# Optimization experiments

Hardware: AMD Instinct MI355X
Metric: run time of the kernel (lower is better)

The kernel has to match this reference:

```python
import jax, jax.numpy as jnp
import numpy as np

B, T, E, D, A, H, C, K = 32, 1500, 512, 512, 512, 4, 10, 201
SHARPENING = 1.0


def setup_inputs() -> dict:
    key = jax.random.key(0)
    ks = jax.random.split(key, 11)
    def w(k, shape, fan_in):
        return jax.random.normal(k, shape, jnp.float32) / np.sqrt(fan_in).astype(np.float32)
    return {
        "enc_out": jax.random.normal(ks[0], (B, T, E), jnp.float32),
        "x_lens": jax.random.randint(ks[1], (B,), T // 2, T + 1),
        "dec_out": jax.random.normal(ks[2], (B, 1, D), jnp.float32),
        # previous-step attention weights: a valid distribution over T per head
        "aw_step": jax.nn.softmax(jax.random.normal(ks[3], (B, T, H), jnp.float32), axis=1),
        "w_enc": w(ks[4], (H, E, A), E),   # per-head LinearND(enc->att)
        "b_enc": jnp.zeros((H, A), jnp.float32),
        "w_dec": w(ks[5], (H, D, A), D),   # per-head LinearND(dec->att), no bias
        "w_conv": w(ks[6], (H, C, A), C),  # per-head LinearND(conv_ch->att), no bias
        "conv_k": w(ks[7], (H * C, 1, K), K),  # grouped 1D conv kernels (O,I,K), groups=H
        "v": w(ks[8], (H, A), A),          # per-head LinearND(att->1), no bias
        "w_mha": w(ks[9], (H * E, E), H * E),
        "b_mha": jnp.zeros((E,), jnp.float32),
    }


def reference(enc_out, x_lens, dec_out, aw_step, w_enc, b_enc, w_dec, w_conv, conv_k, v, w_mha, b_mha):
    b, t, e = enc_out.shape
    h = aw_step.shape[-1]
    c = w_conv.shape[1]
    k = conv_k.shape[-1]
    # enc_out_a: per-head encoder projection [B,T,H,A]
    enc_a = jnp.einsum('bte,hea->btha', enc_out, w_enc) + b_enc
    # decoder projection, broadcast over time [B,1,H,A]
    dec_a = jnp.einsum('bd,hda->bha', dec_out[:, 0], w_dec)[:, None]
    # location features: grouped 1D conv over previous attention weights
    aw_t = jnp.transpose(aw_step, (0, 2, 1))  # [B,H,T]
    conv = jax.lax.conv_general_dilated(
        aw_t, conv_k, window_strides=(1,), padding=[(k // 2, k // 2)],
        dimension_numbers=('NCH', 'OIH', 'NCH'), feature_group_count=h)  # [B,H*C,T]
    conv = conv.reshape(b, h, c, t).transpose(0, 3, 1, 2)  # [B,T,H,C]
    conv_a = jnp.einsum('bthc,hca->btha', conv, w_conv)
    # additive energy [B,T,H]
    energy = jnp.einsum('btha,ha->bth', jnp.tanh(enc_a + dec_a + conv_a), v)
    # original code multiplies energy by mask (1 valid, -1024 padded) then sharpening
    mask = jnp.where(jnp.arange(t)[None, :] < x_lens[:, None], 1.0, -1024.0).astype(energy.dtype)
    energy = energy * mask[:, :, None] * SHARPENING
    aw = jax.nn.softmax(energy, axis=1)  # softmax over time per head
    # per-head context, concatenated along feature dim -> [B,1,H*E]
    ctx = jnp.einsum('bte,bth->bhe', enc_out, aw).reshape(b, 1, h * e)
    ctx = ctx @ w_mha + b_mha  # [B,1,E]
    return ctx, aw
```

## Files before the change

kernel.cpp:

```cpp
#include <hip/hip_runtime.h>
#include <hip/hip_bf16.h>

#define BB 32
#define TT 1500
#define TP 1536
#define EE 512
#define HH 4
#define AA 512
#define NN 2048
#define CC 10
#define KCONV 201
#define KAUG 576

typedef __attribute__((ext_vector_type(8))) __bf16 bf16x8;
typedef __attribute__((ext_vector_type(4))) float f32x4;

__device__ __forceinline__ unsigned short f2bf(float x) {
    unsigned int u = __float_as_uint(x);
    u = (u + 0x7fffu + ((u >> 16) & 1u)) >> 16;
    return (unsigned short)u;
}
__device__ __forceinline__ float bf2f(unsigned short u) {
    return __uint_as_float(((unsigned int)u) << 16);
}
__device__ __forceinline__ void glds16(const void* g, void* l) {
    __builtin_amdgcn_global_load_lds(
        (const __attribute__((address_space(1))) unsigned int*)g,
        (__attribute__((address_space(3))) unsigned int*)l, 16, 0, 0);
}
__device__ __forceinline__ float tanh_fast(float x) {
    float e = __expf(x * 2.0f);
    return fmaf(-2.0f, __builtin_amdgcn_rcpf(e + 1.0f), 1.0f);
}

#define PREP_DEC0   0
#define PREP_CONV0  1024
#define PREP_WT0    8704
#define PREP_PAD0   13312
#define PREP_ENC0   20404
#define PREP_TOTAL  44404

__global__ __launch_bounds__(256) void k_prep(
    const float* __restrict__ enc, const int* __restrict__ xl,
    const float* __restrict__ dec_out, const float* __restrict__ aw_step,
    const float* __restrict__ w_enc, const float* __restrict__ b_enc,
    const float* __restrict__ w_dec, const float* __restrict__ w_conv,
    const float* __restrict__ conv_k,
    unsigned short* __restrict__ Whi, unsigned short* __restrict__ Wlo,
    unsigned short* __restrict__ Ahi, unsigned short* __restrict__ Alo,
    float* __restrict__ dec_a) {
    __shared__ float sbuf[456 + KCONV];
    const int bid = blockIdx.x;
    const int tid = threadIdx.x;

    if (bid < PREP_CONV0) {
        const int b  = bid >> 5;
        const int n0 = (bid & 31) * 64;
        const int n  = n0 + (tid & 63);
        const int dg = tid >> 6;
        const int h  = n >> 9, a = n & 511;
        const float* dp = dec_out + (size_t)b * 512 + dg * 128;
        const float* wp = w_dec + ((size_t)h * 512 + dg * 128) * 512 + a;
        float acc = 0.f;
#pragma unroll 8
        for (int d = 0; d < 128; ++d) acc += dp[d] * wp[(size_t)d * 512];
        sbuf[tid] = acc;
        __syncthreads();
        if (tid < 64) {
            float tot = sbuf[tid] + sbuf[tid + 64] + sbuf[tid + 128] + sbuf[tid + 192];
            dec_a[(size_t)b * NN + n0 + tid] = b_enc[n0 + tid] + tot;
        }
    } else if (bid < PREP_WT0) {
        int r = bid - PREP_CONV0;
        const int tch = r % 6;
        const int hc  = (r / 6) % 40;
        const int b   = r / 240;
        const int h   = hc / 10;
        const int t0  = tch * 256;
        float* sAw = sbuf;
        float* sK  = sbuf + 456;
        for (int i = tid; i < 456; i += 256) {
            int ts = t0 - 100 + i;
            sAw[i] = (ts >= 0 && ts < TT) ? aw_step[((size_t)b * TT + ts) * HH + h] : 0.f;
        }
        if (tid < KCONV) sK[tid] = conv_k[(size_t)hc * KCONV + tid];
        __syncthreads();
        int t = t0 + tid;
        if (t < TT) {
            float acc = 0.f;
            for (int k = 0; k < KCONV; ++k) acc += sAw[tid + k] * sK[k];
            size_t o = ((size_t)b * TP + t) * KAUG + 512 + hc;
            unsigned short hi = f2bf(acc);
            Ahi[o] = hi; Alo[o] = f2bf(acc - bf2f(hi));
        }
    } else if (bid < PREP_PAD0) {
        int idx = (bid - PREP_WT0) * 256 + tid;
        int n = idx / KAUG, k = idx % KAUG;
        int h = n >> 9, a = n & 511;
        float val = 0.f;
        if (k < 512) {
            val = w_enc[((size_t)h * 512 + k) * 512 + a];
        } else if (k < 552) {
            int j = k - 512; int h2 = j / 10, c = j % 10;
            if (h2 == h) val = w_conv[((size_t)h * 10 + c) * 512 + a];
        }
        unsigned short hi = f2bf(val);
        Whi[idx] = hi;
        Wlo[idx] = f2bf(val - bf2f(hi));
    } else if (bid < PREP_ENC0) {
        int idx = (bid - PREP_PAD0) * 256 + tid;
        const int tot1 = BB * 36 * KAUG;
        const int tot2 = BB * TT * 24;
        size_t o;
        if (idx < tot1) {
            int b = idx / (36 * KAUG); int r2 = idx % (36 * KAUG);
            int t = 1500 + r2 / KAUG;  int k = r2 % KAUG;
            o = ((size_t)b * TP + t) * KAUG + k;
        } else if (idx < tot1 + tot2) {
            int j = idx - tot1;
            int b = j / (TT * 24); int r2 = j % (TT * 24);
            int t = r2 / 24;       int k = 552 + r2 % 24;
            o = ((size_t)b * TP + t) * KAUG + k;
        } else return;
        Ahi[o] = 0; Alo[o] = 0;
    } else {
        long idx = (long)(bid - PREP_ENC0) * 256 + tid;
        if (idx >= 6144000L) return;
        long f = idx * 4;
        int b = (int)(f / 768000);
        int r2 = (int)(f % 768000);
        int t = r2 >> 9, e = r2 & 511;
        float4 vv = *reinterpret_cast<const float4*>(enc + f);
        ushort4 h4;
        h4.x = f2bf(vv.x); h4.y = f2bf(vv.y); h4.z = f2bf(vv.z); h4.w = f2bf(vv.w);
        size_t o = ((size_t)b * TP + t) * KAUG + e;
        *reinterpret_cast<ushort4*>(Ahi + o) = h4;
        if (((t & ~127) + 128) > xl[b]) {
            ushort4 l4;
            l4.x = f2bf(vv.x - bf2f(h4.x));
            l4.y = f2bf(vv.y - bf2f(h4.y));
            l4.z = f2bf(vv.z - bf2f(h4.z));
            l4.w = f2bf(vv.w - bf2f(h4.w));
            *reinterpret_cast<ushort4*>(Alo + o) = l4;
        }
    }
}

__global__ __launch_bounds__(256, 3) void k_gemm(
    const unsigned short* __restrict__ Ahi, const unsigned short* __restrict__ Alo,
    const unsigned short* __restrict__ Whi, const unsigned short* __restrict__ Wlo,
    const float* __restrict__ dec_a, const float* __restrict__ vvec,
    const int* __restrict__ xl, float* __restrict__ energy) {
    __shared__ unsigned short lsA[3][4096];
    __shared__ unsigned short lsB[3][4096];
    const int bid = blockIdx.x;
    const int g = ((bid >> 7) << 3) + (bid & 7);
    const int ntile = (bid >> 3) & 15;
    const int b = g / 12, mtile = g % 12;
    const int m0 = mtile * 128, n0 = ntile * 128;
    const int xlen = xl[b];
    const int nk = (m0 + 128 <= xlen) ? 18 : 54;

    const int tid = threadIdx.x;
    const int lane = tid & 63, wave = tid >> 6;
    const int wm = wave >> 1, wn = wave & 1;

    f32x4 acc[4][4];
#pragma unroll
    for (int i = 0; i < 4; i++)
#pragma unroll
        for (int j = 0; j < 4; j++) acc[i][j] = (f32x4){0.f, 0.f, 0.f, 0.f};

    const int row = tid >> 2;
    const int ko  = ((tid & 3) ^ ((tid >> 3) & 3)) * 8;
    const size_t abase = ((size_t)b * TP + m0 + row) * KAUG + ko;
    const size_t bbase = ((size_t)n0 + row) * KAUG + ko;
    const int l1 = tid * 8;
    const int l2 = l1 + 2048;
    const int ar = wm * 64, br = wn * 64;
    const int fo = (lane & 15) * 32 + (((lane >> 4) ^ ((lane >> 1) & 3)) * 8);

    auto stage = [&](int t, int buf) {
        const int seg = (t >= 36) ? 2 : ((t >= 18) ? 1 : 0);
        const int k0 = (t - seg * 18) * 32;
        const unsigned short* Ap = (seg == 2) ? Alo : Ahi;
        const unsigned short* Bp = (seg == 1) ? Wlo : Whi;
        glds16(Ap + abase + k0,                     &lsA[buf][l1]);
        glds16(Ap + abase + k0 + (size_t)64 * KAUG, &lsA[buf][l2]);
        glds16(Bp + bbase + k0,                     &lsB[buf][l1]);
        glds16(Bp + bbase + k0 + (size_t)64 * KAUG, &lsB[buf][l2]);
    };
    auto compute = [&](int buf) {
        bf16x8 ah[4], bh[4];
#pragma unroll
        for (int i = 0; i < 4; i++) {
            ah[i] = *(const bf16x8*)&lsA[buf][(ar + i * 16) * 32 + fo];
            bh[i] = *(const bf16x8*)&lsB[buf][(br + i * 16) * 32 + fo];
        }
        __builtin_amdgcn_s_setprio(1);
#pragma unroll
        for (int i = 0; i < 4; i++)
#pragma unroll
            for (int j = 0; j < 4; j++)
                acc[i][j] = __builtin_amdgcn_mfma_f32_16x16x32_bf16(ah[i], bh[j], acc[i][j], 0, 0, 0);
        __builtin_amdgcn_s_setprio(0);
    };

    stage(0, 0);
    stage(1, 1);
    int bc = 0, bp = 2;
    for (int t = 0; t < nk - 1; ++t) {
        asm volatile("s_waitcnt vmcnt(4)" ::: "memory");
        __builtin_amdgcn_s_barrier();
        __builtin_amdgcn_sched_barrier(0);
        if (t + 2 < nk) stage(t + 2, bp);
        __builtin_amdgcn_sched_barrier(0);
        compute(bc);
        __builtin_amdgcn_sched_barrier(0);
        bc = (bc == 2) ? 0 : bc + 1;
        bp = (bp == 2) ? 0 : bp + 1;
    }
    asm volatile("s_waitcnt vmcnt(0)" ::: "memory");
    __builtin_amdgcn_s_barrier();
    __builtin_amdgcn_sched_barrier(0);
    compute(bc);

    const int h = ntile >> 2;
    const int kg = lane >> 4;
    float dv[4], vv[4];
#pragma unroll
    for (int j = 0; j < 4; j++) {
        int ng = n0 + wn * 64 + j * 16 + (lane & 15);
        dv[j] = dec_a[(size_t)b * NN + ng];
        vv[j] = vvec[ng];
    }
#pragma unroll
    for (int i = 0; i < 4; i++) {
        float part[4] = {0.f, 0.f, 0.f, 0.f};
#pragma unroll
        for (int j = 0; j < 4; j++)
#pragma unroll
            for (int r = 0; r < 4; r++)
                part[r] += tanh_fast(acc[i][j][r] + dv[j]) * vv[j];
#pragma unroll
        for (int r = 0; r < 4; r++) {
            float s = part[r];
            s += __shfl_xor(s, 1, 64);
            s += __shfl_xor(s, 2, 64);
            s += __shfl_xor(s, 4, 64);
            s += __shfl_xor(s, 8, 64);
            if ((lane & 15) == 0) {
                int t = m0 + wm * 64 + i * 16 + kg * 4 + r;
                if (t < TT)
                    atomicAdd(&energy[((size_t)b * HH + h) * TP + t], s);
            }
        }
    }
}

__global__ __launch_bounds__(512) void k_softmax(const float* __restrict__ energy,
                                                 const int* __restrict__ x_lens,
                                                 float* __restrict__ aw) {
    const int b = blockIdx.x >> 2, h = blockIdx.x & 3;
    const int tid = threadIdx.x;
    __shared__ float sE[TT];
    __shared__ float red[512];
    const int xlen = x_lens[b];
    float lmax = -3.4e38f;
    for (int t = tid; t < TT; t += 512) {
        float e = energy[((size_t)b * HH + h) * TP + t];
        float m = (t < xlen) ? e : e * -1024.0f;
        sE[t] = m;
        lmax = fmaxf(lmax, m);
    }
    red[tid] = lmax; __syncthreads();
    for (int s = 256; s > 0; s >>= 1) { if (tid < s) red[tid] = fmaxf(red[tid], red[tid + s]); __syncthreads(); }
    float mx = red[0]; __syncthreads();
    float lsum = 0.f;
    for (int t = tid; t < TT; t += 512) {
        float ex = expf(sE[t] - mx);
        sE[t] = ex; lsum += ex;
    }
    red[tid] = lsum; __syncthreads();
    for (int s = 256; s > 0; s >>= 1) { if (tid < s) red[tid] += red[tid + s]; __syncthreads(); }
    float sum = red[0];
    for (int t = tid; t < TT; t += 512)
        aw[((size_t)b * TT + t) * HH + h] = sE[t] / sum;
}

__global__ __launch_bounds__(512) void k_ctx(const float* __restrict__ enc,
                                             const float* __restrict__ aw,
                                             float* __restrict__ ctx_h) {
    const int chunk = blockIdx.x, b = blockIdx.y;
    const int t0 = chunk * 64;
    const int nt = (TT - t0 < 64) ? (TT - t0) : 64;
    __shared__ float sA[64 * 4];
    const int tid = threadIdx.x;
    for (int i = tid; i < nt * 4; i += 512)
        sA[i] = aw[((size_t)b * TT + t0) * HH + i];
    __syncthreads();
    float a0 = 0.f, a1 = 0.f, a2 = 0.f, a3 = 0.f;
    const float* ep = enc + ((size_t)b * TT + t0) * EE + tid;
    if (nt == 64) {
#pragma unroll 8
        for (int tt = 0; tt < 64; ++tt) {
            float ev = ep[(size_t)tt * EE];
            a0 += sA[tt * 4 + 0] * ev; a1 += sA[tt * 4 + 1] * ev;
            a2 += sA[tt * 4 + 2] * ev; a3 += sA[tt * 4 + 3] * ev;
        }
    } else {
        for (int tt = 0; tt < nt; ++tt) {
            float ev = ep[(size_t)tt * EE];
            a0 += sA[tt * 4 + 0] * ev; a1 += sA[tt * 4 + 1] * ev;
            a2 += sA[tt * 4 + 2] * ev; a3 += sA[tt * 4 + 3] * ev;
        }
    }
    atomicAdd(&ctx_h[((size_t)b * HH + 0) * EE + tid], a0);
    atomicAdd(&ctx_h[((size_t)b * HH + 1) * EE + tid], a1);
    atomicAdd(&ctx_h[((size_t)b * HH + 2) * EE + tid], a2);
    atomicAdd(&ctx_h[((size_t)b * HH + 3) * EE + tid], a3);
}

__global__ __launch_bounds__(256) void k_mha(const float* __restrict__ ctx_h,
                                             const float* __restrict__ w_mha,
                                             const float* __restrict__ b_mha,
                                             float* __restrict__ out) {
    __shared__ float sred[256];
    const int tid = threadIdx.x;
    const int b  = blockIdx.x >> 2;
    const int eo = ((blockIdx.x & 3) << 7) + (tid & 127);
    const int kg = tid >> 7;
    const float* c = ctx_h + (size_t)b * NN + kg * 1024;
    const float* w = w_mha + ((size_t)kg * 1024) * EE + eo;
    float acc = 0.f;
#pragma unroll 8
    for (int k = 0; k < 1024; ++k) acc += c[k] * w[(size_t)k * EE];
    sred[tid] = acc;
    __syncthreads();
    if (tid < 128)
        out[(size_t)b * EE + eo] = b_mha[eo] + sred[tid] + sred[tid + 128];
}

extern "C" void kernel_launch(void* const* d_in, const int* in_sizes, int n_in,
                              void* d_out, int out_size, void* d_ws, size_t ws_size,
                              hipStream_t stream) {
    (void)in_sizes; (void)n_in; (void)out_size;
    const float* enc    = (const float*)d_in[0];
    const int*   xlen   = (const int*)d_in[1];
    const float* dec    = (const float*)d_in[2];
    const float* aw_in  = (const float*)d_in[3];
    const float* w_enc  = (const float*)d_in[4];
    const float* b_enc  = (const float*)d_in[5];
    const float* w_dec  = (const float*)d_in[6];
    const float* w_conv = (const float*)d_in[7];
    const float* convk  = (const float*)d_in[8];
    const float* v      = (const float*)d_in[9];
    const float* w_mha  = (const float*)d_in[10];
    const float* b_mha  = (const float*)d_in[11];
    float* out = (float*)d_out;

    char* ws = (char*)d_ws;
    unsigned short* Whi = (unsigned short*)ws;
    unsigned short* Wlo = Whi + (size_t)NN * KAUG;
    unsigned short* Ahi = (unsigned short*)(ws + 4718592);
    unsigned short* Alo = Ahi + (size_t)BB * TP * KAUG;
    float* dec_a  = (float*)(ws + 117964800);
    float* energy = (float*)(ws + 118226944);
    float* ctx_h  = (float*)(ws + 119013376);
    (void)ws_size;

    hipMemsetAsync(energy, 0, 786432 + 262144, stream);

    k_prep<<<dim3(PREP_TOTAL), 256, 0, stream>>>(enc, xlen, dec, aw_in, w_enc, b_enc,
                                                 w_dec, w_conv, convk,
                                                 Whi, Wlo, Ahi, Alo, dec_a);
    k_gemm<<<dim3(6144), 256, 0, stream>>>(Ahi, Alo, Whi, Wlo, dec_a, v, xlen, energy);
    k_softmax<<<dim3(BB * HH), 512, 0, stream>>>(energy, xlen, out + 16384);
    k_ctx <<<dim3(24, BB), 512, 0, stream>>>(enc, out + 16384, ctx_h);
    k_mha <<<dim3(128), 256, 0, stream>>>(ctx_h, w_mha, b_mha, out);
}
```

Measured before the change: 595.2 us.

## Enlarge GEMM tiles to 256x256 with 8 waves and interleaved loads

The energy GEMM moves from 128x128 tiles with 4 waves to 256x256 tiles with 512 threads, so each wave holds an 8x4 block of MFMA accumulators. The K-loop is restructured so the global-to-LDS stages are spread between four MFMA phases rather than issued as one batch, and block order is remapped so heavy tail tiles (the last M tiles) are scheduled first. The low-precision correction region widens from 128-row to 256-row granularity, so more rows take the 54-step path. Fewer blocks and more data reuse per tile are traded against higher register/LDS pressure, lower occupancy and more wasted work on partial tiles.

Measured after the change: 623.4 us. 1.05x slower.

```diff
diff --git a/kernel.cpp b/kernel.cpp
--- a/kernel.cpp
+++ b/kernel.cpp
@@ -135,7 +135,7 @@
         h4.x = f2bf(vv.x); h4.y = f2bf(vv.y); h4.z = f2bf(vv.z); h4.w = f2bf(vv.w);
         size_t o = ((size_t)b * TP + t) * KAUG + e;
         *reinterpret_cast<ushort4*>(Ahi + o) = h4;
-        if (((t & ~127) + 128) > xl[b]) {
+        if (((t & ~255) + 256) > xl[b]) {
             ushort4 l4;
             l4.x = f2bf(vv.x - bf2f(h4.x));
             l4.y = f2bf(vv.y - bf2f(h4.y));
@@ -146,86 +146,112 @@
     }
 }
 
-__global__ __launch_bounds__(256, 3) void k_gemm(
+__global__ __launch_bounds__(512, 2) void k_gemm(
     const unsigned short* __restrict__ Ahi, const unsigned short* __restrict__ Alo,
     const unsigned short* __restrict__ Whi, const unsigned short* __restrict__ Wlo,
     const float* __restrict__ dec_a, const float* __restrict__ vvec,
     const int* __restrict__ xl, float* __restrict__ energy) {
-    __shared__ unsigned short lsA[3][4096];
-    __shared__ unsigned short lsB[3][4096];
+    __shared__ unsigned short lsA[3][8192];
+    __shared__ unsigned short lsB[3][8192];
     const int bid = blockIdx.x;
-    const int g = ((bid >> 7) << 3) + (bid & 7);
-    const int ntile = (bid >> 3) & 15;
-    const int b = g / 12, mtile = g % 12;
-    const int m0 = mtile * 128, n0 = ntile * 128;
+    const int ntile = bid & 7;
+    const int rest = bid >> 3;
+    const int mtile = 5 - (rest >> 5);
+    const int b = rest & 31;
+    const int m0 = mtile * 256, n0 = ntile * 256;
     const int xlen = xl[b];
-    const int nk = (m0 + 128 <= xlen) ? 18 : 54;
+    const int nk = (m0 + 256 <= xlen) ? 18 : 54;
 
     const int tid = threadIdx.x;
     const int lane = tid & 63, wave = tid >> 6;
-    const int wm = wave >> 1, wn = wave & 1;
-
-    f32x4 acc[4][4];
-#pragma unroll
-    for (int i = 0; i < 4; i++)
+    const int wm = wave >> 2, wn = wave & 3;
+
+    f32x4 acc[8][4];
+#pragma unroll
+    for (int i = 0; i < 8; i++)
 #pragma unroll
         for (int j = 0; j < 4; j++) acc[i][j] = (f32x4){0.f, 0.f, 0.f, 0.f};
 
-    const int row = tid >> 2;
-    const int ko  = ((tid & 3) ^ ((tid >> 3) & 3)) * 8;
-    const size_t abase = ((size_t)b * TP + m0 + row) * KAUG + ko;
-    const size_t bbase = ((size_t)n0 + row) * KAUG + ko;
-    const int l1 = tid * 8;
-    const int l2 = l1 + 2048;
-    const int ar = wm * 64, br = wn * 64;
-    const int fo = (lane & 15) * 32 + (((lane >> 4) ^ ((lane >> 1) & 3)) * 8);
-
-    auto stage = [&](int t, int buf) {
-        const int seg = (t >= 36) ? 2 : ((t >= 18) ? 1 : 0);
-        const int k0 = (t - seg * 18) * 32;
-        const unsigned short* Ap = (seg == 2) ? Alo : Ahi;
-        const unsigned short* Bp = (seg == 1) ? Wlo : Whi;
-        glds16(Ap + abase + k0,                     &lsA[buf][l1]);
-        glds16(Ap + abase + k0 + (size_t)64 * KAUG, &lsA[buf][l2]);
-        glds16(Bp + bbase + k0,                     &lsB[buf][l1]);
-        glds16(Bp + bbase + k0 + (size_t)64 * KAUG, &lsB[buf][l2]);
-    };
-    auto compute = [&](int buf) {
-        bf16x8 ah[4], bh[4];
-#pragma unroll
-        for (int i = 0; i < 4; i++) {
-            ah[i] = *(const bf16x8*)&lsA[buf][(ar + i * 16) * 32 + fo];
-            bh[i] = *(const bf16x8*)&lsB[buf][(br + i * 16) * 32 + fo];
-        }
-        __builtin_amdgcn_s_setprio(1);
-#pragma unroll
-        for (int i = 0; i < 4; i++)
-#pragma unroll
-            for (int j = 0; j < 4; j++)
-                acc[i][j] = __builtin_amdgcn_mfma_f32_16x16x32_bf16(ah[i], bh[j], acc[i][j], 0, 0, 0);
-        __builtin_amdgcn_s_setprio(0);
-    };
-
-    stage(0, 0);
-    stage(1, 1);
-    int bc = 0, bp = 2;
-    for (int t = 0; t < nk - 1; ++t) {
-        asm volatile("s_waitcnt vmcnt(4)" ::: "memory");
-        __builtin_amdgcn_s_barrier();
-        __builtin_amdgcn_sched_barrier(0);
-        if (t + 2 < nk) stage(t + 2, bp);
-        __builtin_amdgcn_sched_barrier(0);
-        compute(bc);
-        __builtin_amdgcn_sched_barrier(0);
-        bc = (bc == 2) ? 0 : bc + 1;
-        bp = (bp == 2) ? 0 : bp + 1;
-    }
-    asm volatile("s_waitcnt vmcnt(0)" ::: "memory");
+    const int r = tid >> 2;
+    const int rowP2 = r + (r & 64);
+    const int ko = ((tid & 3) ^ ((r >> 1) & 3)) * 8;
+    const size_t abase = ((size_t)b * TP + m0 + rowP2) * KAUG + ko;
+    const size_t bbase = ((size_t)n0 + r) * KAUG + ko;
+    const int ldstA = rowP2 * 32 + (tid & 3) * 8;
+    const int ldstB = tid * 8;
+    const int fc = ((lane >> 4) ^ ((lane >> 1) & 3)) * 8;
+    const int arow0 = wm * 128 + (lane & 15);
+    const int brow0 = wn * 64 + (lane & 15);
+
+#define STG0(BUF, BP, K0) glds16((BP) + bbase + (K0), &lsB[BUF][ldstB])
+#define STG1(BUF, BP, K0) glds16((BP) + bbase + (size_t)128 * KAUG + (K0), &lsB[BUF][ldstB + 4096])
+#define STG2(BUF, AP, K0) glds16((AP) + abase + (K0), &lsA[BUF][ldstA])
+#define STG3(BUF, AP, K0) glds16((AP) + abase + (size_t)64 * KAUG + (K0), &lsA[BUF][ldstA + 2048])
+#define MFMA4(AF, AI) \
+    acc[AI][0] = __builtin_amdgcn_mfma_f32_16x16x32_bf16(AF, bfr0, acc[AI][0], 0, 0, 0); \
+    acc[AI][1] = __builtin_amdgcn_mfma_f32_16x16x32_bf16(AF, bfr1, acc[AI][1], 0, 0, 0); \
+    acc[AI][2] = __builtin_amdgcn_mfma_f32_16x16x32_bf16(AF, bfr2, acc[AI][2], 0, 0, 0); \
+    acc[AI][3] = __builtin_amdgcn_mfma_f32_16x16x32_bf16(AF, bfr3, acc[AI][3], 0, 0, 0);
+#define PHASE(P) { \
+    bf16x8 a0 = *(const bf16x8*)&lA[(arow0 + (2 * (P)) * 16) * 32 + fc]; \
+    bf16x8 a1 = *(const bf16x8*)&lA[(arow0 + (2 * (P) + 1) * 16) * 32 + fc]; \
+    __builtin_amdgcn_s_setprio(1); \
+    MFMA4(a0, 2 * (P)); \
+    MFMA4(a1, 2 * (P) + 1); \
+    __builtin_amdgcn_s_setprio(0); }
+
+    STG0(0, Whi, 0); STG1(0, Whi, 0); STG2(0, Ahi, 0); STG3(0, Ahi, 0);
+    STG0(1, Whi, 32); STG1(1, Whi, 32); STG2(1, Ahi, 32); STG3(1, Ahi, 32);
+    asm volatile("s_waitcnt vmcnt(4)" ::: "memory");
     __builtin_amdgcn_s_barrier();
     __builtin_amdgcn_sched_barrier(0);
-    compute(bc);
-
-    const int h = ntile >> 2;
+
+    int bc = 0;
+    for (int s = 0; s < nk; ++s) {
+        const int sp = s + 2;
+        const bool st = sp < nk;
+        const int bp2 = (bc + 2 >= 3) ? bc - 1 : bc + 2;
+        const unsigned short* ApN = Ahi;
+        const unsigned short* BpN = Whi;
+        int k0n = 0;
+        if (st) {
+            const int seg = (sp >= 36) ? 2 : ((sp >= 18) ? 1 : 0);
+            k0n = (sp - seg * 18) * 32;
+            if (seg == 2) ApN = Alo;
+            if (seg == 1) BpN = Wlo;
+        }
+        const unsigned short* lA = lsA[bc];
+        const unsigned short* lB = lsB[bc];
+
+        if (st) STG0(bp2, BpN, k0n);
+        bf16x8 bfr0 = *(const bf16x8*)&lB[(brow0 + 0) * 32 + fc];
+        bf16x8 bfr1 = *(const bf16x8*)&lB[(brow0 + 16) * 32 + fc];
+        bf16x8 bfr2 = *(const bf16x8*)&lB[(brow0 + 32) * 32 + fc];
+        bf16x8 bfr3 = *(const bf16x8*)&lB[(brow0 + 48) * 32 + fc];
+        PHASE(0)
+        if (st) STG1(bp2, BpN, k0n);
+        PHASE(1)
+        if (st) STG2(bp2, ApN, k0n);
+        PHASE(2)
+        if (st) STG3(bp2, ApN, k0n);
+        PHASE(3)
+
+        if (s < nk - 1) {
+            if (st) asm volatile("s_waitcnt vmcnt(4)" ::: "memory");
+            else    asm volatile("s_waitcnt vmcnt(0)" ::: "memory");
+            __builtin_amdgcn_s_barrier();
+            __builtin_amdgcn_sched_barrier(0);
+        }
+        bc = (bc == 2) ? 0 : bc + 1;
+    }
+#undef STG0
+#undef STG1
+#undef STG2
+#undef STG3
+#undef MFMA4
+#undef PHASE
+
+    const int h = ntile >> 1;
     const int kg = lane >> 4;
     float dv[4], vv[4];
 #pragma unroll
@@ -235,22 +261,22 @@
         vv[j] = vvec[ng];
     }
 #pragma unroll
-    for (int i = 0; i < 4; i++) {
+    for (int i = 0; i < 8; i++) {
         float part[4] = {0.f, 0.f, 0.f, 0.f};
 #pragma unroll
         for (int j = 0; j < 4; j++)
 #pragma unroll
-            for (int r = 0; r < 4; r++)
-                part[r] += tanh_fast(acc[i][j][r] + dv[j]) * vv[j];
-#pragma unroll
-        for (int r = 0; r < 4; r++) {
-            float s = part[r];
+            for (int rr = 0; rr < 4; rr++)
+                part[rr] += tanh_fast(acc[i][j][rr] + dv[j]) * vv[j];
+#pragma unroll
+        for (int rr = 0; rr < 4; rr++) {
+            float s = part[rr];
             s += __shfl_xor(s, 1, 64);
             s += __shfl_xor(s, 2, 64);
             s += __shfl_xor(s, 4, 64);
             s += __shfl_xor(s, 8, 64);
             if ((lane & 15) == 0) {
-                int t = m0 + wm * 64 + i * 16 + kg * 4 + r;
+                int t = m0 + wm * 128 + i * 16 + kg * 4 + rr;
                 if (t < TT)
                     atomicAdd(&energy[((size_t)b * HH + h) * TP + t], s);
             }
@@ -374,7 +400,7 @@
     k_prep<<<dim3(PREP_TOTAL), 256, 0, stream>>>(enc, xlen, dec, aw_in, w_enc, b_enc,
                                                  w_dec, w_conv, convk,
                                                  Whi, Wlo, Ahi, Alo, dec_a);
-    k_gemm<<<dim3(6144), 256, 0, stream>>>(Ahi, Alo, Whi, Wlo, dec_a, v, xlen, energy);
+    k_gemm<<<dim3(1536), 512, 0, stream>>>(Ahi, Alo, Whi, Wlo, dec_a, v, xlen, energy);
     k_softmax<<<dim3(BB * HH), 512, 0, stream>>>(energy, xlen, out + 16384);
     k_ctx <<<dim3(24, BB), 512, 0, stream>>>(enc, out + 16384, ctx_h);
     k_mha <<<dim3(128), 256, 0, stream>>>(ctx_h, w_mha, b_mha, out);
```

## Stage GEMM tiles through registers with LDS double buffering; schedule heavy tiles first

Applied to the files above, without the earlier changes.

Drops the triple-buffered direct global-to-LDS loads in the energy GEMM. Tiles are now loaded into registers, written to a swizzled two-buffer LDS ring, and computed in a ping-pong loop that waits on lgkmcnt plus a barrier rather than on vmcnt. This halves LDS use per block and decouples global-load latency from the LDS write, at the cost of extra VGPRs and explicit LDS stores. It also reverses the time-tile order within each batch so the partially padded tiles, which run the longer 54-step K loop, are dispatched first to shrink the tail.

Measured after the change: 627.9 us. 5.5% more time.

```diff
diff --git a/kernel.cpp b/kernel.cpp
--- a/kernel.cpp
+++ b/kernel.cpp
@@ -22,11 +22,6 @@
 }
 __device__ __forceinline__ float bf2f(unsigned short u) {
     return __uint_as_float(((unsigned int)u) << 16);
-}
-__device__ __forceinline__ void glds16(const void* g, void* l) {
-    __builtin_amdgcn_global_load_lds(
-        (const __attribute__((address_space(1))) unsigned int*)g,
-        (__attribute__((address_space(3))) unsigned int*)l, 16, 0, 0);
 }
 __device__ __forceinline__ float tanh_fast(float x) {
     float e = __expf(x * 2.0f);
@@ -151,12 +146,13 @@
     const unsigned short* __restrict__ Whi, const unsigned short* __restrict__ Wlo,
     const float* __restrict__ dec_a, const float* __restrict__ vvec,
     const int* __restrict__ xl, float* __restrict__ energy) {
-    __shared__ unsigned short lsA[3][4096];
-    __shared__ unsigned short lsB[3][4096];
+    __shared__ unsigned short lsA[2][4096];
+    __shared__ unsigned short lsB[2][4096];
     const int bid = blockIdx.x;
     const int g = ((bid >> 7) << 3) + (bid & 7);
     const int ntile = (bid >> 3) & 15;
-    const int b = g / 12, mtile = g % 12;
+    const int b = g / 12;
+    const int mtile = 11 - (g % 12);
     const int m0 = mtile * 128, n0 = ntile * 128;
     const int xlen = xl[b];
     const int nk = (m0 + 128 <= xlen) ? 18 : 54;
@@ -171,59 +167,82 @@
 #pragma unroll
         for (int j = 0; j < 4; j++) acc[i][j] = (f32x4){0.f, 0.f, 0.f, 0.f};
 
-    const int row = tid >> 2;
-    const int ko  = ((tid & 3) ^ ((tid >> 3) & 3)) * 8;
-    const size_t abase = ((size_t)b * TP + m0 + row) * KAUG + ko;
-    const size_t bbase = ((size_t)n0 + row) * KAUG + ko;
-    const int l1 = tid * 8;
-    const int l2 = l1 + 2048;
+    const int srow = tid >> 1;
+    const int sc0  = (tid & 1) * 2;
+    const int ssw  = (srow >> 1) & 3;
+    const size_t aoff = ((size_t)b * TP + m0 + srow) * KAUG + sc0 * 8;
+    const size_t boff = ((size_t)n0 + srow) * KAUG + sc0 * 8;
+    const int wA0 = srow * 32 + ((sc0 ^ ssw) * 8);
+    const int wA1 = srow * 32 + (((sc0 + 1) ^ ssw) * 8);
+
     const int ar = wm * 64, br = wn * 64;
     const int fo = (lane & 15) * 32 + (((lane >> 4) ^ ((lane >> 1) & 3)) * 8);
 
-    auto stage = [&](int t, int buf) {
-        const int seg = (t >= 36) ? 2 : ((t >= 18) ? 1 : 0);
-        const int k0 = (t - seg * 18) * 32;
-        const unsigned short* Ap = (seg == 2) ? Alo : Ahi;
-        const unsigned short* Bp = (seg == 1) ? Wlo : Whi;
-        glds16(Ap + abase + k0,                     &lsA[buf][l1]);
-        glds16(Ap + abase + k0 + (size_t)64 * KAUG, &lsA[buf][l2]);
-        glds16(Bp + bbase + k0,                     &lsB[buf][l1]);
-        glds16(Bp + bbase + k0 + (size_t)64 * KAUG, &lsB[buf][l2]);
-    };
-    auto compute = [&](int buf) {
-        bf16x8 ah[4], bh[4];
-#pragma unroll
-        for (int i = 0; i < 4; i++) {
-            ah[i] = *(const bf16x8*)&lsA[buf][(ar + i * 16) * 32 + fo];
-            bh[i] = *(const bf16x8*)&lsB[buf][(br + i * 16) * 32 + fo];
-        }
-        __builtin_amdgcn_s_setprio(1);
-#pragma unroll
-        for (int i = 0; i < 4; i++)
-#pragma unroll
-            for (int j = 0; j < 4; j++)
-                acc[i][j] = __builtin_amdgcn_mfma_f32_16x16x32_bf16(ah[i], bh[j], acc[i][j], 0, 0, 0);
-        __builtin_amdgcn_s_setprio(0);
-    };
-
-    stage(0, 0);
-    stage(1, 1);
-    int bc = 0, bp = 2;
-    for (int t = 0; t < nk - 1; ++t) {
-        asm volatile("s_waitcnt vmcnt(4)" ::: "memory");
-        __builtin_amdgcn_s_barrier();
+    float4 rA00, rA01, rB00, rB01;
+    float4 rA10, rA11, rB10, rB11;
+
+#define PLANES(SP, APV, BPV, K0V) \
+    const unsigned short* APV = ((SP) >= 36) ? Alo : Ahi; \
+    const unsigned short* BPV = (((SP) >= 18) && ((SP) < 36)) ? Wlo : Whi; \
+    const int K0V = ((SP) - (((SP) >= 36) ? 36 : (((SP) >= 18) ? 18 : 0))) * 32;
+
+#define ISSUE(SP, R0, R1, R2, R3) { \
+    PLANES(SP, Ap_, Bp_, k0_) \
+    R0 = *(const float4*)(Ap_ + aoff + k0_); \
+    R1 = *(const float4*)(Ap_ + aoff + k0_ + 8); \
+    R2 = *(const float4*)(Bp_ + boff + k0_); \
+    R3 = *(const float4*)(Bp_ + boff + k0_ + 8); }
+
+#define WRITE(BUF, R0, R1, R2, R3) { \
+    *(float4*)&lsA[BUF][wA0] = R0; \
+    *(float4*)&lsA[BUF][wA1] = R1; \
+    *(float4*)&lsB[BUF][wA0] = R2; \
+    *(float4*)&lsB[BUF][wA1] = R3; }
+
+#define COMPUTE(BUF) { \
+    bf16x8 ah[4], bh[4]; \
+    _Pragma("unroll") \
+    for (int i = 0; i < 4; i++) { \
+        ah[i] = *(const bf16x8*)&lsA[BUF][(ar + i * 16) * 32 + fo]; \
+        bh[i] = *(const bf16x8*)&lsB[BUF][(br + i * 16) * 32 + fo]; \
+    } \
+    __builtin_amdgcn_s_setprio(1); \
+    _Pragma("unroll") \
+    for (int i = 0; i < 4; i++) \
+    _Pragma("unroll") \
+        for (int j = 0; j < 4; j++) \
+            acc[i][j] = __builtin_amdgcn_mfma_f32_16x16x32_bf16(ah[i], bh[j], acc[i][j], 0, 0, 0); \
+    __builtin_amdgcn_s_setprio(0); }
+
+#define SEAL() { \
+    asm volatile("s_waitcnt lgkmcnt(0)" ::: "memory"); \
+    __builtin_amdgcn_s_barrier(); \
+    __builtin_amdgcn_sched_barrier(0); }
+
+    ISSUE(0, rA00, rA01, rB00, rB01);
+    ISSUE(1, rA10, rA11, rB10, rB11);
+    WRITE(0, rA00, rA01, rB00, rB01);
+    SEAL();
+
+    for (int t = 0; t < nk; t += 2) {
+        if (t + 2 < nk) ISSUE(t + 2, rA00, rA01, rB00, rB01);
         __builtin_amdgcn_sched_barrier(0);
-        if (t + 2 < nk) stage(t + 2, bp);
+        WRITE(1, rA10, rA11, rB10, rB11);
+        COMPUTE(0);
+        SEAL();
+        if (t + 3 < nk) ISSUE(t + 3, rA10, rA11, rB10, rB11);
         __builtin_amdgcn_sched_barrier(0);
-        compute(bc);
-        __builtin_amdgcn_sched_barrier(0);
-        bc = (bc == 2) ? 0 : bc + 1;
-        bp = (bp == 2) ? 0 : bp + 1;
-    }
-    asm volatile("s_waitcnt vmcnt(0)" ::: "memory");
-    __builtin_amdgcn_s_barrier();
-    __builtin_amdgcn_sched_barrier(0);
-    compute(bc);
+        if (t + 2 < nk) {
+            WRITE(0, rA00, rA01, rB00, rB01);
+        }
+        COMPUTE(1);
+        if (t + 2 < nk) SEAL();
+    }
+#undef PLANES
+#undef ISSUE
+#undef WRITE
+#undef COMPUTE
+#undef SEAL
 
     const int h = ntile >> 2;
     const int kg = lane >> 4;
@@ -250,9 +269,9 @@
             s += __shfl_xor(s, 4, 64);
             s += __shfl_xor(s, 8, 64);
             if ((lane & 15) == 0) {
-                int t = m0 + wm * 64 + i * 16 + kg * 4 + r;
-                if (t < TT)
-                    atomicAdd(&energy[((size_t)b * HH + h) * TP + t], s);
+                int tt = m0 + wm * 64 + i * 16 + kg * 4 + r;
+                if (tt < TT)
+                    atomicAdd(&energy[((size_t)b * HH + h) * TP + tt], s);
             }
         }
     }
```

## Enlarge GEMM tiles to 256x256 with 8 waves and phased ping-pong pipeline

Applied to the files above, without the earlier changes.

Rewrites the energy GEMM to use 256x256 output tiles per 512-thread block with BK=64, double-buffered LDS, and a four-phase schedule that interleaves global-to-LDS loads with MFMA quadrants. Tail tiles are scheduled first so the slow three-segment tiles start early. The decoder projection in prep is restructured so each block computes 8 batches per weight load, cutting block count. The intent is higher arithmetic intensity and fewer redundant global loads of A and W. In exchange, the coarser 256-row tiles compute the low-precision correction over more rows, the residual-writing threshold widens to match, and register pressure is higher.

New measurement: 581.8 us. 1.02x faster.

```diff
diff --git a/kernel.cpp b/kernel.cpp
--- a/kernel.cpp
+++ b/kernel.cpp
@@ -34,11 +34,11 @@
 }
 
 #define PREP_DEC0   0
-#define PREP_CONV0  1024
-#define PREP_WT0    8704
-#define PREP_PAD0   13312
-#define PREP_ENC0   20404
-#define PREP_TOTAL  44404
+#define PREP_CONV0  32
+#define PREP_WT0    7712
+#define PREP_PAD0   12320
+#define PREP_ENC0   19412
+#define PREP_TOTAL  43412
 
 __global__ __launch_bounds__(256) void k_prep(
     const float* __restrict__ enc, const int* __restrict__ xl,
@@ -54,22 +54,22 @@
     const int tid = threadIdx.x;
 
     if (bid < PREP_CONV0) {
-        const int b  = bid >> 5;
-        const int n0 = (bid & 31) * 64;
-        const int n  = n0 + (tid & 63);
-        const int dg = tid >> 6;
-        const int h  = n >> 9, a = n & 511;
-        const float* dp = dec_out + (size_t)b * 512 + dg * 128;
-        const float* wp = w_dec + ((size_t)h * 512 + dg * 128) * 512 + a;
-        float acc = 0.f;
-#pragma unroll 8
-        for (int d = 0; d < 128; ++d) acc += dp[d] * wp[(size_t)d * 512];
-        sbuf[tid] = acc;
-        __syncthreads();
-        if (tid < 64) {
-            float tot = sbuf[tid] + sbuf[tid + 64] + sbuf[tid + 128] + sbuf[tid + 192];
-            dec_a[(size_t)b * NN + n0 + tid] = b_enc[n0 + tid] + tot;
-        }
+        const int h = bid >> 3;
+        const int a = ((bid & 7) << 6) + (tid & 63);
+        const int bg = tid >> 6;
+        float acc[8] = {0.f, 0.f, 0.f, 0.f, 0.f, 0.f, 0.f, 0.f};
+        const float* wp = w_dec + (size_t)h * 512 * 512 + a;
+#pragma unroll 4
+        for (int d = 0; d < 512; ++d) {
+            float w = wp[(size_t)d * 512];
+#pragma unroll
+            for (int q = 0; q < 8; ++q)
+                acc[q] += dec_out[(size_t)(bg * 8 + q) * 512 + d] * w;
+        }
+        const float be = b_enc[h * 512 + a];
+#pragma unroll
+        for (int q = 0; q < 8; ++q)
+            dec_a[(size_t)(bg * 8 + q) * NN + h * 512 + a] = be + acc[q];
     } else if (bid < PREP_WT0) {
         int r = bid - PREP_CONV0;
         const int tch = r % 6;
@@ -135,7 +135,7 @@
         h4.x = f2bf(vv.x); h4.y = f2bf(vv.y); h4.z = f2bf(vv.z); h4.w = f2bf(vv.w);
         size_t o = ((size_t)b * TP + t) * KAUG + e;
         *reinterpret_cast<ushort4*>(Ahi + o) = h4;
-        if (((t & ~127) + 128) > xl[b]) {
+        if (((t & ~255) + 256) > xl[b]) {
             ushort4 l4;
             l4.x = f2bf(vv.x - bf2f(h4.x));
             l4.y = f2bf(vv.y - bf2f(h4.y));
@@ -146,86 +146,168 @@
     }
 }
 
-__global__ __launch_bounds__(256, 3) void k_gemm(
+__global__ __launch_bounds__(512, 2) void k_gemm(
     const unsigned short* __restrict__ Ahi, const unsigned short* __restrict__ Alo,
     const unsigned short* __restrict__ Whi, const unsigned short* __restrict__ Wlo,
     const float* __restrict__ dec_a, const float* __restrict__ vvec,
     const int* __restrict__ xl, float* __restrict__ energy) {
-    __shared__ unsigned short lsA[3][4096];
-    __shared__ unsigned short lsB[3][4096];
+    __shared__ unsigned short lsA[2][16384];
+    __shared__ unsigned short lsB[2][16384];
     const int bid = blockIdx.x;
-    const int g = ((bid >> 7) << 3) + (bid & 7);
-    const int ntile = (bid >> 3) & 15;
-    const int b = g / 12, mtile = g % 12;
-    const int m0 = mtile * 128, n0 = ntile * 128;
+    const int ntile = bid & 7;
+    const int rest = bid >> 3;
+    const int b = rest & 31;
+    const int mtile = 5 - (rest >> 5);
+    const int m0 = mtile * 256, n0 = ntile * 256;
     const int xlen = xl[b];
-    const int nk = (m0 + 128 <= xlen) ? 18 : 54;
+    const int nkt = (m0 + 256 <= xlen) ? 9 : 27;
+    const int nIter = nkt >> 1;
 
     const int tid = threadIdx.x;
     const int lane = tid & 63, wave = tid >> 6;
-    const int wm = wave >> 1, wn = wave & 1;
-
-    f32x4 acc[4][4];
-#pragma unroll
-    for (int i = 0; i < 4; i++)
+    const int wm = wave >> 2, wn = wave & 3;
+
+    f32x4 acc[8][4];
+#pragma unroll
+    for (int i = 0; i < 8; i++)
 #pragma unroll
         for (int j = 0; j < 4; j++) acc[i][j] = (f32x4){0.f, 0.f, 0.f, 0.f};
 
-    const int row = tid >> 2;
-    const int ko  = ((tid & 3) ^ ((tid >> 3) & 3)) * 8;
-    const size_t abase = ((size_t)b * TP + m0 + row) * KAUG + ko;
-    const size_t bbase = ((size_t)n0 + row) * KAUG + ko;
-    const int l1 = tid * 8;
-    const int l2 = l1 + 2048;
-    const int ar = wm * 64, br = wn * 64;
-    const int fo = (lane & 15) * 32 + (((lane >> 4) ^ ((lane >> 1) & 3)) * 8);
-
-    auto stage = [&](int t, int buf) {
-        const int seg = (t >= 36) ? 2 : ((t >= 18) ? 1 : 0);
-        const int k0 = (t - seg * 18) * 32;
-        const unsigned short* Ap = (seg == 2) ? Alo : Ahi;
-        const unsigned short* Bp = (seg == 1) ? Wlo : Whi;
-        glds16(Ap + abase + k0,                     &lsA[buf][l1]);
-        glds16(Ap + abase + k0 + (size_t)64 * KAUG, &lsA[buf][l2]);
-        glds16(Bp + bbase + k0,                     &lsB[buf][l1]);
-        glds16(Bp + bbase + k0 + (size_t)64 * KAUG, &lsB[buf][l2]);
+    const int srow = tid >> 3;
+    const int cg8 = ((tid & 7) ^ (srow & 7)) << 3;
+    const size_t aRow0 = ((size_t)b * TP + m0 + srow) * KAUG + cg8;
+    const size_t bRow0 = ((size_t)n0 + srow) * KAUG + cg8;
+
+    auto stgA = [&](int buf, int half, const unsigned short* Ap, int k0) {
+        const unsigned short* s = Ap + aRow0 + (size_t)half * 128 * KAUG + k0;
+        unsigned short* d = &lsA[buf][half * 8192 + tid * 8];
+        glds16(s, d);
+        glds16(s + (size_t)64 * KAUG, d + 4096);
     };
-    auto compute = [&](int buf) {
-        bf16x8 ah[4], bh[4];
-#pragma unroll
-        for (int i = 0; i < 4; i++) {
-            ah[i] = *(const bf16x8*)&lsA[buf][(ar + i * 16) * 32 + fo];
-            bh[i] = *(const bf16x8*)&lsB[buf][(br + i * 16) * 32 + fo];
-        }
+    auto stgB = [&](int buf, int half, const unsigned short* Bp, int k0) {
+        const unsigned short* s = Bp + bRow0 + (size_t)half * 128 * KAUG + k0;
+        unsigned short* d = &lsB[buf][half * 8192 + tid * 8];
+        glds16(s, d);
+        glds16(s + (size_t)64 * KAUG, d + 4096);
+    };
+
+    const int l15 = lane & 15, lk = lane >> 4, lsw = lane & 7;
+    const int aoff = (((wm << 7) + l15) << 6);
+    const int boff = (((wn << 6) + l15) << 6);
+    const int ac0 = ((lk ^ lsw) << 3);
+    const int ac1 = (((4 | lk) ^ lsw) << 3);
+
+    bf16x8 aLo[4][2], aHi[4][2], bLo[2][2], bHi[2][2];
+
+#define RDALO(P) { _Pragma("unroll") for (int i = 0; i < 4; ++i) { \
+    aLo[i][0] = *(const bf16x8*)&lsA[P][aoff + i * 1024 + ac0]; \
+    aLo[i][1] = *(const bf16x8*)&lsA[P][aoff + i * 1024 + ac1]; } }
+#define RDAHI(P) { _Pragma("unroll") for (int i = 0; i < 4; ++i) { \
+    aHi[i][0] = *(const bf16x8*)&lsA[P][aoff + (i + 4) * 1024 + ac0]; \
+    aHi[i][1] = *(const bf16x8*)&lsA[P][aoff + (i + 4) * 1024 + ac1]; } }
+#define RDBLO(P) { _Pragma("unroll") for (int j = 0; j < 2; ++j) { \
+    bLo[j][0] = *(const bf16x8*)&lsB[P][boff + j * 1024 + ac0]; \
+    bLo[j][1] = *(const bf16x8*)&lsB[P][boff + j * 1024 + ac1]; } }
+#define RDBHI(P) { _Pragma("unroll") for (int j = 0; j < 2; ++j) { \
+    bHi[j][0] = *(const bf16x8*)&lsB[P][boff + (j + 2) * 1024 + ac0]; \
+    bHi[j][1] = *(const bf16x8*)&lsB[P][boff + (j + 2) * 1024 + ac1]; } }
+#define MFQ(AARR, IOFF, BARR, JOFF) { \
+    _Pragma("unroll") for (int i = 0; i < 4; ++i) \
+    _Pragma("unroll") for (int j = 0; j < 2; ++j) { \
+        acc[(IOFF) + i][(JOFF) + j] = __builtin_amdgcn_mfma_f32_16x16x32_bf16(AARR[i][0], BARR[j][0], acc[(IOFF) + i][(JOFF) + j], 0, 0, 0); \
+        acc[(IOFF) + i][(JOFF) + j] = __builtin_amdgcn_mfma_f32_16x16x32_bf16(AARR[i][1], BARR[j][1], acc[(IOFF) + i][(JOFF) + j], 0, 0, 0); } }
+#define PH_ENTER() { __builtin_amdgcn_s_barrier(); \
+    asm volatile("s_waitcnt lgkmcnt(0)" ::: "memory"); \
+    __builtin_amdgcn_sched_barrier(0); __builtin_amdgcn_s_setprio(1); }
+#define PH_EXIT()  { __builtin_amdgcn_s_setprio(0); __builtin_amdgcn_s_barrier(); \
+    __builtin_amdgcn_sched_barrier(0); }
+
+    stgA(0, 0, Ahi, 0); stgA(0, 1, Ahi, 0);
+    stgB(0, 0, Whi, 0); stgB(0, 1, Whi, 0);
+    stgA(1, 0, Ahi, 64); stgA(1, 1, Ahi, 64);
+    __builtin_amdgcn_sched_barrier(0);
+    asm volatile("s_waitcnt vmcnt(4)" ::: "memory");
+    __builtin_amdgcn_s_barrier();
+    __builtin_amdgcn_sched_barrier(0);
+
+    for (int it = 0; it < nIter; ++it) {
+        const int kt0 = it << 1;
+        const int ktA = kt0 + 1, ktB = kt0 + 2, ktC = kt0 + 3;
+        const unsigned short* BpA = (ktA >= 9 && ktA < 18) ? Wlo : Whi;
+        const int kA = ((ktA >= 18) ? ktA - 18 : (ktA >= 9) ? ktA - 9 : ktA) * 64;
+        const unsigned short* ApB = (ktB >= 18) ? Alo : Ahi;
+        const unsigned short* BpB = (ktB >= 9 && ktB < 18) ? Wlo : Whi;
+        const int kB = ((ktB >= 18) ? ktB - 18 : (ktB >= 9) ? ktB - 9 : ktB) * 64;
+        const unsigned short* ApC = (ktC >= 18) ? Alo : Ahi;
+        const int kC = ((ktC >= 18) ? ktC - 18 : (ktC >= 9) ? ktC - 9 : ktC) * 64;
+        const bool notLast = (it != nIter - 1);
+
+        RDALO(0); RDBLO(0);
+        stgB(1, 0, BpA, kA);
+        PH_ENTER(); MFQ(aLo, 0, bLo, 0); PH_EXIT();
+        RDAHI(0);
+        stgB(1, 1, BpA, kA);
+        PH_ENTER(); MFQ(aHi, 4, bLo, 0); PH_EXIT();
+        RDBHI(0);
+        stgA(0, 0, ApB, kB);
+        PH_ENTER(); MFQ(aLo, 0, bHi, 2); PH_EXIT();
+        stgA(0, 1, ApB, kB);
+        __builtin_amdgcn_s_barrier();
+        __builtin_amdgcn_sched_barrier(0);
         __builtin_amdgcn_s_setprio(1);
-#pragma unroll
-        for (int i = 0; i < 4; i++)
-#pragma unroll
-            for (int j = 0; j < 4; j++)
-                acc[i][j] = __builtin_amdgcn_mfma_f32_16x16x32_bf16(ah[i], bh[j], acc[i][j], 0, 0, 0);
+        MFQ(aHi, 4, bHi, 2);
         __builtin_amdgcn_s_setprio(0);
-    };
-
-    stage(0, 0);
-    stage(1, 1);
-    int bc = 0, bp = 2;
-    for (int t = 0; t < nk - 1; ++t) {
+        __builtin_amdgcn_sched_barrier(0);
         asm volatile("s_waitcnt vmcnt(4)" ::: "memory");
         __builtin_amdgcn_s_barrier();
         __builtin_amdgcn_sched_barrier(0);
-        if (t + 2 < nk) stage(t + 2, bp);
-        __builtin_amdgcn_sched_barrier(0);
-        compute(bc);
-        __builtin_amdgcn_sched_barrier(0);
-        bc = (bc == 2) ? 0 : bc + 1;
-        bp = (bp == 2) ? 0 : bp + 1;
-    }
+
+        RDALO(1); RDBLO(1);
+        stgB(0, 0, BpB, kB);
+        PH_ENTER(); MFQ(aLo, 0, bLo, 0); PH_EXIT();
+        RDAHI(1);
+        stgB(0, 1, BpB, kB);
+        PH_ENTER(); MFQ(aHi, 4, bLo, 0); PH_EXIT();
+        RDBHI(1);
+        if (notLast) stgA(1, 0, ApC, kC);
+        PH_ENTER(); MFQ(aLo, 0, bHi, 2); PH_EXIT();
+        if (notLast) stgA(1, 1, ApC, kC);
+        __builtin_amdgcn_s_barrier();
+        __builtin_amdgcn_sched_barrier(0);
+        __builtin_amdgcn_s_setprio(1);
+        MFQ(aHi, 4, bHi, 2);
+        __builtin_amdgcn_s_setprio(0);
+        __builtin_amdgcn_sched_barrier(0);
+        if (notLast) asm volatile("s_waitcnt vmcnt(4)" ::: "memory");
+        __builtin_amdgcn_s_barrier();
+        __builtin_amdgcn_sched_barrier(0);
+    }
+
     asm volatile("s_waitcnt vmcnt(0)" ::: "memory");
     __builtin_amdgcn_s_barrier();
     __builtin_amdgcn_sched_barrier(0);
-    compute(bc);
-
-    const int h = ntile >> 2;
+    RDALO(0); RDBLO(0);
+    asm volatile("s_waitcnt lgkmcnt(0)" ::: "memory");
+    __builtin_amdgcn_sched_barrier(0);
+    MFQ(aLo, 0, bLo, 0);
+    RDAHI(0);
+    asm volatile("s_waitcnt lgkmcnt(0)" ::: "memory");
+    __builtin_amdgcn_sched_barrier(0);
+    MFQ(aHi, 4, bLo, 0);
+    RDBHI(0);
+    asm volatile("s_waitcnt lgkmcnt(0)" ::: "memory");
+    __builtin_amdgcn_sched_barrier(0);
+    MFQ(aLo, 0, bHi, 2);
+    MFQ(aHi, 4, bHi, 2);
+#undef RDALO
+#undef RDAHI
+#undef RDBLO
+#undef RDBHI
+#undef MFQ
+#undef PH_ENTER
+#undef PH_EXIT
+
+    const int h = ntile >> 1;
     const int kg = lane >> 4;
     float dv[4], vv[4];
 #pragma unroll
@@ -235,22 +317,22 @@
         vv[j] = vvec[ng];
     }
 #pragma unroll
-    for (int i = 0; i < 4; i++) {
+    for (int i = 0; i < 8; i++) {
         float part[4] = {0.f, 0.f, 0.f, 0.f};
 #pragma unroll
         for (int j = 0; j < 4; j++)
 #pragma unroll
-            for (int r = 0; r < 4; r++)
-                part[r] += tanh_fast(acc[i][j][r] + dv[j]) * vv[j];
-#pragma unroll
-        for (int r = 0; r < 4; r++) {
-            float s = part[r];
+            for (int rr = 0; rr < 4; rr++)
+                part[rr] += tanh_fast(acc[i][j][rr] + dv[j]) * vv[j];
+#pragma unroll
+        for (int rr = 0; rr < 4; rr++) {
+            float s = part[rr];
             s += __shfl_xor(s, 1, 64);
             s += __shfl_xor(s, 2, 64);
             s += __shfl_xor(s, 4, 64);
             s += __shfl_xor(s, 8, 64);
             if ((lane & 15) == 0) {
-                int t = m0 + wm * 64 + i * 16 + kg * 4 + r;
+                int t = m0 + wm * 128 + i * 16 + kg * 4 + rr;
                 if (t < TT)
                     atomicAdd(&energy[((size_t)b * HH + h) * TP + t], s);
             }
@@ -374,7 +456,7 @@
     k_prep<<<dim3(PREP_TOTAL), 256, 0, stream>>>(enc, xlen, dec, aw_in, w_enc, b_enc,
                                                  w_dec, w_conv, convk,
                                                  Whi, Wlo, Ahi, Alo, dec_a);
-    k_gemm<<<dim3(6144), 256, 0, stream>>>(Ahi, Alo, Whi, Wlo, dec_a, v, xlen, energy);
+    k_gemm<<<dim3(1536), 512, 0, stream>>>(Ahi, Alo, Whi, Wlo, dec_a, v, xlen, energy);
     k_softmax<<<dim3(BB * HH), 512, 0, stream>>>(energy, xlen, out + 16384);
     k_ctx <<<dim3(24, BB), 512, 0, stream>>>(enc, out + 16384, ctx_h);
     k_mha <<<dim3(128), 256, 0, stream>>>(ctx_h, w_mha, b_mha, out);
```
